# Kernel optimization log

Measured on AMD Instinct MI355X. Metric: run time of the kernel, lower is better.

## Reference

```python
import jax, jax.numpy as jnp
import numpy as np

NUM_HEADS = 16
KEY_DIM = 64
NUM_FEATURES = 256
D_MODEL = NUM_HEADS * KEY_DIM
EPS = 1e-6


def softmax_kernel(data, proj):
    # data: [..., N, D], proj: [D, F]
    # Faithful to source: ratio uses proj.shape[0] (=D), matching the TF code.
    data_normalizer = 1.0 / jnp.sqrt(jnp.sqrt(jnp.asarray(data.shape[-1], data.dtype)))
    ratio = 1.0 / jnp.sqrt(jnp.asarray(proj.shape[0], data.dtype))
    data = data_normalizer * data
    data_dash = jnp.einsum('...nd,df->...nf', data, proj)
    diag = jnp.sum(jnp.square(data), axis=-1, keepdims=True)  # [..., N, 1]
    return ratio * (jnp.exp(data_dash - diag / 2.0) + EPS)


def setup_inputs() -> dict:
    key = jax.random.key(0)
    ks = jax.random.split(key, 12)
    B, N = 4, 4096
    s = 1.0 / np.sqrt(D_MODEL)
    inp = {
        'queries': jax.random.normal(ks[0], (B, N, D_MODEL), jnp.float32),
        'keys': jax.random.normal(ks[1], (B, N, D_MODEL), jnp.float32),
        'Wq': jax.random.normal(ks[2], (D_MODEL, D_MODEL), jnp.float32) * s,
        'bq': jnp.zeros((D_MODEL,), jnp.float32),
        'Wk': jax.random.normal(ks[3], (D_MODEL, D_MODEL), jnp.float32) * s,
        'bk': jnp.zeros((D_MODEL,), jnp.float32),
        'Wv': jax.random.normal(ks[4], (D_MODEL, D_MODEL), jnp.float32) * s,
        'bv': jnp.zeros((D_MODEL,), jnp.float32),
        'Wo': jax.random.normal(ks[5], (D_MODEL, D_MODEL), jnp.float32) * s,
        'bo': jnp.zeros((D_MODEL,), jnp.float32),
        # GlorotNormal for [KEY_DIM, NUM_FEATURES]
        'proj': jax.random.normal(ks[6], (KEY_DIM, NUM_FEATURES), jnp.float32)
                * np.sqrt(2.0 / (KEY_DIM + NUM_FEATURES)),
    }
    return inp


def reference(queries, keys, Wq, bq, Wk, bk, Wv, bv, Wo, bo, proj):
    # Original code uses x = queries for q, k, v (self-attention); keys arg unused.
    x = queries
    B, N, _ = x.shape
    H, D = NUM_HEADS, KEY_DIM

    def split_heads(t):
        return t.reshape(B, N, H, D).transpose(0, 2, 1, 3)  # [B,H,N,D]

    q = split_heads(x @ Wq + bq)
    k = split_heads(x @ Wk + bk)
    v = split_heads(x @ Wv + bv)

    q_prime = softmax_kernel(q, proj)  # [B,H,N,F]
    k_prime = softmax_kernel(k, proj)  # [B,H,N,F]

    kv = jnp.einsum('bhnf,bhnd->bhfd', k_prime, v)        # [B,H,F,D]
    qkv = jnp.einsum('bhnf,bhfd->bhnd', q_prime, kv)       # [B,H,N,D]
    k_sum = jnp.sum(k_prime, axis=2)                        # [B,H,F]
    norm = jnp.einsum('bhnf,bhf->bhn', q_prime, k_sum) + EPS
    qkv = qkv / norm[..., None]

    out = qkv.transpose(0, 2, 1, 3).reshape(B, N, H * D)    # [B,N,d_model]
    return out @ Wo + bo
```

## Files before the change

### kernel.cpp

```cpp
#include <hip/hip_runtime.h>

typedef __attribute__((ext_vector_type(8))) short short8;
typedef __attribute__((ext_vector_type(4))) float f32x4;

#define MFMA16 __builtin_amdgcn_mfma_f32_16x16x32_bf16

#define GLOAD16(gp, lp) __builtin_amdgcn_global_load_lds(                      \
    (const __attribute__((address_space(1))) void*)(gp),                       \
    (__attribute__((address_space(3))) void*)(lp), 16, 0, 0)

__device__ __forceinline__ unsigned short f2bf(float f) {
  unsigned int u = __float_as_uint(f);
  unsigned int r = u + 0x7fffu + ((u >> 16) & 1u);
  return (unsigned short)(r >> 16);
}
__device__ __forceinline__ float bf2f(unsigned short h) {
  return __uint_as_float(((unsigned int)h) << 16);
}

__global__ __launch_bounds__(256) void cast_x_kernel(
    const float* __restrict__ in, unsigned short* __restrict__ out, int n4) {
  int i = blockIdx.x * 256 + threadIdx.x;
  if (i >= n4) return;
  float4 v = reinterpret_cast<const float4*>(in)[i];
  ushort4 o;
  o.x = f2bf(v.x); o.y = f2bf(v.y); o.z = f2bf(v.z); o.w = f2bf(v.w);
  reinterpret_cast<ushort4*>(out)[i] = o;
}

__global__ __launch_bounds__(256) void tcast_f32_kernel(
    const float* __restrict__ in, unsigned short* __restrict__ out, int R, int C) {
  __shared__ float t[64][65];
  int c0 = blockIdx.x * 64, r0 = blockIdx.y * 64;
  int tx = threadIdx.x, ty = threadIdx.y;
#pragma unroll
  for (int i = 0; i < 16; ++i)
    t[ty + 4 * i][tx] = in[(size_t)(r0 + ty + 4 * i) * C + c0 + tx];
  __syncthreads();
#pragma unroll
  for (int i = 0; i < 16; ++i)
    out[(size_t)(c0 + ty + 4 * i) * R + r0 + tx] = f2bf(t[tx][ty + 4 * i]);
}

__global__ __launch_bounds__(256) void t_bf16_kernel(
    const unsigned short* __restrict__ in, unsigned short* __restrict__ out, int R, int C) {
  __shared__ unsigned short t[64][66];
  size_t base = (size_t)blockIdx.z * (size_t)R * (size_t)C;
  int c0 = blockIdx.x * 64, r0 = blockIdx.y * 64;
  int tx = threadIdx.x, ty = threadIdx.y;
#pragma unroll
  for (int i = 0; i < 16; ++i)
    t[ty + 4 * i][tx] = in[base + (size_t)(r0 + ty + 4 * i) * C + c0 + tx];
  __syncthreads();
#pragma unroll
  for (int i = 0; i < 16; ++i)
    out[base + (size_t)(c0 + ty + 4 * i) * R + r0 + tx] = t[tx][ty + 4 * i];
}

template <int OUTF>
__global__ __launch_bounds__(256) void gemm_bt_kernel(
    const unsigned short* __restrict__ A,
    const unsigned short* W0, const unsigned short* W1, const unsigned short* W2,
    const float* b0, const float* b1, const float* b2,
    void* o0, void* o1, void* o2) {
  constexpr int KD = 1024, ND = 1024;
  const unsigned short* W = W0; const float* bias = b0; void* op = o0;
  if (blockIdx.z == 1) { W = W1; bias = b1; op = o1; }
  else if (blockIdx.z == 2) { W = W2; bias = b2; op = o2; }

  __shared__ unsigned short lsA[128 * 32];
  __shared__ unsigned short lsB[128 * 32];
  int tid = threadIdx.x;
  int w = tid >> 6, lane = tid & 63;
  int m0 = blockIdx.x * 128, n0 = blockIdx.y * 128;
  int wm = (w >> 1) * 64, wn = (w & 1) * 64;

  int srow0 = (w * 2 + 0) * 16 + (lane >> 2);
  int srow1 = (w * 2 + 1) * 16 + (lane >> 2);
  int scol = (lane & 3) * 8;
  const unsigned short* gA0 = A + (size_t)(m0 + srow0) * KD + scol;
  const unsigned short* gA1 = A + (size_t)(m0 + srow1) * KD + scol;
  const unsigned short* gB0 = W + (size_t)(n0 + srow0) * KD + scol;
  const unsigned short* gB1 = W + (size_t)(n0 + srow1) * KD + scol;
  unsigned short* lA0 = &lsA[(w * 2 + 0) * 512];
  unsigned short* lA1 = &lsA[(w * 2 + 1) * 512];
  unsigned short* lB0 = &lsB[(w * 2 + 0) * 512];
  unsigned short* lB1 = &lsB[(w * 2 + 1) * 512];

  f32x4 acc[4][4];
#pragma unroll
  for (int fm = 0; fm < 4; ++fm)
#pragma unroll
    for (int fn = 0; fn < 4; ++fn) acc[fm][fn] = (f32x4){0.f, 0.f, 0.f, 0.f};

  for (int kt = 0; kt < KD; kt += 32) {
    GLOAD16(gA0 + kt, lA0);
    GLOAD16(gA1 + kt, lA1);
    GLOAD16(gB0 + kt, lB0);
    GLOAD16(gB1 + kt, lB1);
    __syncthreads();
    short8 af[4], bfr[4];
#pragma unroll
    for (int fm = 0; fm < 4; ++fm)
      af[fm] = *reinterpret_cast<const short8*>(
          &lsA[(wm + fm * 16 + (lane & 15)) * 32 + (lane >> 4) * 8]);
#pragma unroll
    for (int fn = 0; fn < 4; ++fn)
      bfr[fn] = *reinterpret_cast<const short8*>(
          &lsB[(wn + fn * 16 + (lane & 15)) * 32 + (lane >> 4) * 8]);
#pragma unroll
    for (int fm = 0; fm < 4; ++fm)
#pragma unroll
      for (int fn = 0; fn < 4; ++fn)
        acc[fm][fn] = MFMA16(af[fm], bfr[fn], acc[fm][fn], 0, 0, 0);
    __syncthreads();
  }

#pragma unroll
  for (int fn = 0; fn < 4; ++fn) {
    int col = n0 + wn + fn * 16 + (lane & 15);
    float bv = bias[col];
#pragma unroll
    for (int fm = 0; fm < 4; ++fm) {
#pragma unroll
      for (int j = 0; j < 4; ++j) {
        int row = m0 + wm + fm * 16 + (lane >> 4) * 4 + j;
        float v = acc[fm][fn][j] + bv;
        if (OUTF)
          reinterpret_cast<float*>(op)[(size_t)row * ND + col] = v;
        else
          reinterpret_cast<unsigned short*>(op)[(size_t)row * ND + col] = f2bf(v);
      }
    }
  }
}

__global__ __launch_bounds__(256) void kv_fused_kernel(
    const unsigned short* __restrict__ K, const unsigned short* __restrict__ PT,
    const unsigned short* __restrict__ VT,
    float* __restrict__ kvp, float* __restrict__ ksp) {
  __shared__ unsigned short kp[256 * 40];
  int s = blockIdx.x, bh = blockIdx.y, b = bh >> 4, h = bh & 15;
  int tid = threadIdx.x, w = tid >> 6, lane = tid & 63;
  int lo = lane & 15, hi = lane >> 4;
  int f0w = w * 64;

  short8 pb[4][2];
#pragma unroll
  for (int fn = 0; fn < 4; ++fn) {
    int f = f0w + fn * 16 + lo;
    pb[fn][0] = *reinterpret_cast<const short8*>(PT + (size_t)f * 64 + hi * 8);
    pb[fn][1] = *reinterpret_cast<const short8*>(PT + (size_t)f * 64 + 32 + hi * 8);
  }
  const unsigned short* vbase[4];
#pragma unroll
  for (int fn = 0; fn < 4; ++fn)
    vbase[fn] = VT + (size_t)(bh * 64 + fn * 16 + lo) * 4096;

  f32x4 acck[4][4];
#pragma unroll
  for (int fm = 0; fm < 4; ++fm)
#pragma unroll
    for (int fn = 0; fn < 4; ++fn) acck[fm][fn] = (f32x4){0.f, 0.f, 0.f, 0.f};
  float ks[4] = {0.f, 0.f, 0.f, 0.f};

  for (int c = 0; c < 16; ++c) {
    int n0 = s * 512 + c * 32;
    const unsigned short* Ab = K + (size_t)(b * 4096 + n0) * 1024 + h * 64;
    short8 af[2][2];
    float dp[2] = {0.f, 0.f};
#pragma unroll
    for (int fm = 0; fm < 2; ++fm)
#pragma unroll
      for (int kt = 0; kt < 2; ++kt) {
        af[fm][kt] = *reinterpret_cast<const short8*>(
            Ab + (size_t)(fm * 16 + lo) * 1024 + kt * 32 + hi * 8);
#pragma unroll
        for (int j = 0; j < 8; ++j) {
          float qv = bf2f((unsigned short)af[fm][kt][j]);
          dp[fm] += qv * qv;
        }
      }
#pragma unroll
    for (int fm = 0; fm < 2; ++fm) {
      dp[fm] += __shfl_xor(dp[fm], 16);
      dp[fm] += __shfl_xor(dp[fm], 32);
    }
    f32x4 accf[2][4];
#pragma unroll
    for (int fm = 0; fm < 2; ++fm)
#pragma unroll
      for (int fn = 0; fn < 4; ++fn) accf[fm][fn] = (f32x4){0.f, 0.f, 0.f, 0.f};
#pragma unroll
    for (int fn = 0; fn < 4; ++fn) {
      accf[0][fn] = MFMA16(af[0][0], pb[fn][0], accf[0][fn], 0, 0, 0);
      accf[0][fn] = MFMA16(af[0][1], pb[fn][1], accf[0][fn], 0, 0, 0);
      accf[1][fn] = MFMA16(af[1][0], pb[fn][0], accf[1][fn], 0, 0, 0);
      accf[1][fn] = MFMA16(af[1][1], pb[fn][1], accf[1][fn], 0, 0, 0);
    }
#pragma unroll
    for (int fm = 0; fm < 2; ++fm)
#pragma unroll
      for (int fn = 0; fn < 4; ++fn)
#pragma unroll
        for (int j = 0; j < 4; ++j) {
          float dg = __shfl(dp[fm], hi * 4 + j);
          float v = 0.125f *
                    (__expf(0.35355339059327373f * accf[fm][fn][j] - 0.0625f * dg) + 1e-6f);
          ks[fn] += v;
          kp[(f0w + fn * 16 + lo) * 40 + fm * 16 + hi * 4 + j] = f2bf(v);
        }
    short8 a2[4], b2[4];
#pragma unroll
    for (int fm = 0; fm < 4; ++fm)
      a2[fm] = *reinterpret_cast<const short8*>(&kp[(f0w + fm * 16 + lo) * 40 + hi * 8]);
#pragma unroll
    for (int fn = 0; fn < 4; ++fn)
      b2[fn] = *reinterpret_cast<const short8*>(vbase[fn] + n0 + hi * 8);
#pragma unroll
    for (int fm = 0; fm < 4; ++fm)
#pragma unroll
      for (int fn = 0; fn < 4; ++fn)
        acck[fm][fn] = MFMA16(a2[fm], b2[fn], acck[fm][fn], 0, 0, 0);
  }
#pragma unroll
  for (int fn = 0; fn < 4; ++fn) {
    float v = ks[fn];
    v += __shfl_xor(v, 16);
    v += __shfl_xor(v, 32);
    if (hi == 0)
      ksp[(size_t)(s * 64 + bh) * 256 + f0w + fn * 16 + lo] = v;
  }
#pragma unroll
  for (int fm = 0; fm < 4; ++fm)
#pragma unroll
    for (int fn = 0; fn < 4; ++fn)
#pragma unroll
      for (int j = 0; j < 4; ++j)
        kvp[((size_t)(s * 64 + bh) * 256 + f0w + fm * 16 + hi * 4 + j) * 64 + fn * 16 + lo] =
            acck[fm][fn][j];
}

__global__ __launch_bounds__(256) void kvred_kernel(
    const float* __restrict__ kvp, const float* __restrict__ ksp,
    unsigned short* __restrict__ kvT, float* __restrict__ ksum) {
  int bh = blockIdx.x, tid = threadIdx.x;
  for (int i = tid; i < 64 * 256; i += 256) {
    int f = i >> 6, d = i & 63;
    float sum = 0.f;
#pragma unroll
    for (int s = 0; s < 8; ++s)
      sum += kvp[((size_t)(s * 64 + bh) * 256 + f) * 64 + d];
    kvT[(size_t)(bh * 64 + d) * 256 + f] = f2bf(sum);
  }
  {
    float t = 0.f;
#pragma unroll
    for (int s = 0; s < 8; ++s) t += ksp[(size_t)(s * 64 + bh) * 256 + tid];
    ksum[bh * 256 + tid] = t;
  }
}

__global__ __launch_bounds__(256) void qkv_fused_kernel(
    const unsigned short* __restrict__ Q, const unsigned short* __restrict__ PT,
    const unsigned short* __restrict__ KVT, const float* __restrict__ KSUM,
    unsigned short* __restrict__ Y) {
  __shared__ unsigned short qp[128 * 256];
  int bh = blockIdx.y, b = bh >> 4, h = bh & 15;
  int t0 = blockIdx.x * 128;
  int tid = threadIdx.x, w = tid >> 6, lane = tid & 63;
  int lo = lane & 15, hi = lane >> 4;
  int r0 = w * 32;
  const unsigned short* Ab = Q + (size_t)(b * 4096 + t0 + r0) * 1024 + h * 64;

  float ksr[16];
#pragma unroll
  for (int fn = 0; fn < 16; ++fn) ksr[fn] = KSUM[bh * 256 + fn * 16 + lo];

  short8 af[2][2];
  float dp[2] = {0.f, 0.f};
#pragma unroll
  for (int fm = 0; fm < 2; ++fm)
#pragma unroll
    for (int kt = 0; kt < 2; ++kt) {
      af[fm][kt] = *reinterpret_cast<const short8*>(
          Ab + (size_t)(fm * 16 + lo) * 1024 + kt * 32 + hi * 8);
#pragma unroll
      for (int j = 0; j < 8; ++j) {
        float qv = bf2f((unsigned short)af[fm][kt][j]);
        dp[fm] += qv * qv;
      }
    }
#pragma unroll
  for (int fm = 0; fm < 2; ++fm) {
    dp[fm] += __shfl_xor(dp[fm], 16);
    dp[fm] += __shfl_xor(dp[fm], 32);
  }

  float np[2][4] = {{0.f, 0.f, 0.f, 0.f}, {0.f, 0.f, 0.f, 0.f}};
#pragma unroll
  for (int hf = 0; hf < 2; ++hf) {
    f32x4 accf[2][8];
#pragma unroll
    for (int fm = 0; fm < 2; ++fm)
#pragma unroll
      for (int fn = 0; fn < 8; ++fn) accf[fm][fn] = (f32x4){0.f, 0.f, 0.f, 0.f};
#pragma unroll
    for (int fn = 0; fn < 8; ++fn) {
      int f = (hf * 8 + fn) * 16 + lo;
      short8 pb0 = *reinterpret_cast<const short8*>(PT + (size_t)f * 64 + hi * 8);
      short8 pb1 = *reinterpret_cast<const short8*>(PT + (size_t)f * 64 + 32 + hi * 8);
      accf[0][fn] = MFMA16(af[0][0], pb0, accf[0][fn], 0, 0, 0);
      accf[0][fn] = MFMA16(af[0][1], pb1, accf[0][fn], 0, 0, 0);
      accf[1][fn] = MFMA16(af[1][0], pb0, accf[1][fn], 0, 0, 0);
      accf[1][fn] = MFMA16(af[1][1], pb1, accf[1][fn], 0, 0, 0);
    }
#pragma unroll
    for (int fm = 0; fm < 2; ++fm)
#pragma unroll
      for (int fn = 0; fn < 8; ++fn)
#pragma unroll
        for (int j = 0; j < 4; ++j) {
          float dg = __shfl(dp[fm], hi * 4 + j);
          float v = 0.125f *
                    (__expf(0.35355339059327373f * accf[fm][fn][j] - 0.0625f * dg) + 1e-6f);
          np[fm][j] += v * ksr[hf * 8 + fn];
          int row = r0 + fm * 16 + hi * 4 + j;
          int f = (hf * 8 + fn) * 16 + lo;
          int byt = (row * 512 + f * 2) ^ ((row & 7) << 4);
          *reinterpret_cast<unsigned short*>(reinterpret_cast<char*>(qp) + byt) = f2bf(v);
        }
  }
#pragma unroll
  for (int fm = 0; fm < 2; ++fm)
#pragma unroll
    for (int j = 0; j < 4; ++j) {
      np[fm][j] += __shfl_xor(np[fm][j], 1);
      np[fm][j] += __shfl_xor(np[fm][j], 2);
      np[fm][j] += __shfl_xor(np[fm][j], 4);
      np[fm][j] += __shfl_xor(np[fm][j], 8);
    }
  f32x4 acco[2][4];
#pragma unroll
  for (int fm = 0; fm < 2; ++fm)
#pragma unroll
    for (int fn = 0; fn < 4; ++fn) acco[fm][fn] = (f32x4){0.f, 0.f, 0.f, 0.f};
#pragma unroll
  for (int kt2 = 0; kt2 < 8; ++kt2) {
    short8 a2[2], b2[4];
#pragma unroll
    for (int fm = 0; fm < 2; ++fm) {
      int row = r0 + fm * 16 + lo;
      int byt = (row * 512 + kt2 * 64 + hi * 16) ^ ((row & 7) << 4);
      a2[fm] = *reinterpret_cast<const short8*>(reinterpret_cast<char*>(qp) + byt);
    }
#pragma unroll
    for (int fn = 0; fn < 4; ++fn)
      b2[fn] = *reinterpret_cast<const short8*>(
          KVT + (size_t)(bh * 64 + fn * 16 + lo) * 256 + kt2 * 32 + hi * 8);
#pragma unroll
    for (int fm = 0; fm < 2; ++fm)
#pragma unroll
      for (int fn = 0; fn < 4; ++fn)
        acco[fm][fn] = MFMA16(a2[fm], b2[fn], acco[fm][fn], 0, 0, 0);
  }
#pragma unroll
  for (int fm = 0; fm < 2; ++fm)
#pragma unroll
    for (int j = 0; j < 4; ++j) {
      float nv = np[fm][j] + 1e-6f;
      int row = b * 4096 + t0 + r0 + fm * 16 + hi * 4 + j;
#pragma unroll
      for (int fn = 0; fn < 4; ++fn)
        Y[(size_t)row * 1024 + h * 64 + fn * 16 + lo] = f2bf(acco[fm][fn][j] / nv);
    }
}

extern "C" void kernel_launch(void* const* d_in, const int* in_sizes, int n_in,
                              void* d_out, int out_size, void* d_ws, size_t ws_size,
                              hipStream_t stream) {
  (void)in_sizes; (void)n_in; (void)out_size; (void)ws_size;
  const float* x    = (const float*)d_in[0];
  const float* Wq   = (const float*)d_in[2];
  const float* bq   = (const float*)d_in[3];
  const float* Wk   = (const float*)d_in[4];
  const float* bk   = (const float*)d_in[5];
  const float* Wv   = (const float*)d_in[6];
  const float* bv   = (const float*)d_in[7];
  const float* Wo   = (const float*)d_in[8];
  const float* bo   = (const float*)d_in[9];
  const float* proj = (const float*)d_in[10];
  float* out = (float*)d_out;

  constexpr size_t SZ_XB = (size_t)16384 * 1024 * 2;
  constexpr size_t SZ_W  = (size_t)1024 * 1024 * 2;
  constexpr size_t SZ_PT = (size_t)256 * 64 * 2;

  char* p = (char*)d_ws;
  size_t off = 0;
  char* a_xb  = p + off; off += SZ_XB;
  char* a_WqT = p + off; off += SZ_W;
  char* a_WkT = p + off; off += SZ_W;
  char* a_WvT = p + off; off += SZ_W;
  char* a_WoT = p + off; off += SZ_W;
  char* a_pT  = p + off; off += SZ_PT;
  char* a_qb  = p + off; off += SZ_XB;
  char* a_kb  = p + off; off += SZ_XB;
  char* a_ksp  = p + off; off += (size_t)8 * 64 * 256 * 4;
  char* a_kvT  = p + off; off += (size_t)64 * 64 * 256 * 2;
  char* a_ksum = p + off; off += (size_t)64 * 256 * 4;

  char* a_kvp = a_xb;
  char* a_y = a_kb;
  char* a_vb = (char*)d_out;
  char* a_vT = (char*)d_out + SZ_XB;

  dim3 tb(64, 4);

  cast_x_kernel<<<16384, 256, 0, stream>>>(x, (unsigned short*)a_xb, 16384 * 1024 / 4);
  tcast_f32_kernel<<<dim3(16, 16), tb, 0, stream>>>(Wq, (unsigned short*)a_WqT, 1024, 1024);
  tcast_f32_kernel<<<dim3(16, 16), tb, 0, stream>>>(Wk, (unsigned short*)a_WkT, 1024, 1024);
  tcast_f32_kernel<<<dim3(16, 16), tb, 0, stream>>>(Wv, (unsigned short*)a_WvT, 1024, 1024);
  tcast_f32_kernel<<<dim3(16, 16), tb, 0, stream>>>(Wo, (unsigned short*)a_WoT, 1024, 1024);
  tcast_f32_kernel<<<dim3(4, 1), tb, 0, stream>>>(proj, (unsigned short*)a_pT, 64, 256);

  gemm_bt_kernel<0><<<dim3(128, 8, 3), 256, 0, stream>>>(
      (unsigned short*)a_xb,
      (unsigned short*)a_WqT, (unsigned short*)a_WkT, (unsigned short*)a_WvT,
      bq, bk, bv, a_qb, a_kb, a_vb);

  t_bf16_kernel<<<dim3(16, 64, 4), tb, 0, stream>>>(
      (unsigned short*)a_vb, (unsigned short*)a_vT, 4096, 1024);

  kv_fused_kernel<<<dim3(8, 64), 256, 0, stream>>>(
      (unsigned short*)a_kb, (unsigned short*)a_pT, (unsigned short*)a_vT,
      (float*)a_kvp, (float*)a_ksp);
  kvred_kernel<<<64, 256, 0, stream>>>(
      (float*)a_kvp, (float*)a_ksp, (unsigned short*)a_kvT, (float*)a_ksum);

  qkv_fused_kernel<<<dim3(32, 64), 256, 0, stream>>>(
      (unsigned short*)a_qb, (unsigned short*)a_pT, (unsigned short*)a_kvT,
      (float*)a_ksum, (unsigned short*)a_y);

  gemm_bt_kernel<1><<<dim3(128, 8, 1), 256, 0, stream>>>(
      (unsigned short*)a_y,
      (unsigned short*)a_WoT, nullptr, nullptr,
      bo, nullptr, nullptr, out, nullptr, nullptr);
}
```

Measured before the change: 356.4 us.

## Rewrite projection GEMMs as 256x256 double-buffered tiles with swizzled LDS

Replaces the 128x128, single-buffered GEMM with a 256x256 tile per 512-thread block and a K-step of 64. LDS is double-buffered so the next tile's global->LDS loads overlap the current MFMAs. An XOR swizzle on LDS chunks avoids bank conflicts, and explicit waitcnt, barriers and setprio control the schedule. This is meant to raise operand reuse and hide memory latency in the QKV and output projections. The cost is much more LDS (128 KB) and registers per block, so occupancy drops, and only 256 or 768 blocks are launched.

```diff
diff --git a/kernel.cpp b/kernel.cpp
--- a/kernel.cpp
+++ b/kernel.cpp
@@ -58,80 +58,112 @@
 }
 
 template <int OUTF>
-__global__ __launch_bounds__(256) void gemm_bt_kernel(
+__global__ __launch_bounds__(512) void gemm256_kernel(
     const unsigned short* __restrict__ A,
     const unsigned short* W0, const unsigned short* W1, const unsigned short* W2,
     const float* b0, const float* b1, const float* b2,
     void* o0, void* o1, void* o2) {
-  constexpr int KD = 1024, ND = 1024;
+  constexpr int KD = 1024, ND = 1024, NT = KD / 64;
   const unsigned short* W = W0; const float* bias = b0; void* op = o0;
   if (blockIdx.z == 1) { W = W1; bias = b1; op = o1; }
   else if (blockIdx.z == 2) { W = W2; bias = b2; op = o2; }
 
-  __shared__ unsigned short lsA[128 * 32];
-  __shared__ unsigned short lsB[128 * 32];
+  __shared__ unsigned short lsA[2][16384];
+  __shared__ unsigned short lsB[2][16384];
   int tid = threadIdx.x;
   int w = tid >> 6, lane = tid & 63;
-  int m0 = blockIdx.x * 128, n0 = blockIdx.y * 128;
-  int wm = (w >> 1) * 64, wn = (w & 1) * 64;
-
-  int srow0 = (w * 2 + 0) * 16 + (lane >> 2);
-  int srow1 = (w * 2 + 1) * 16 + (lane >> 2);
-  int scol = (lane & 3) * 8;
-  const unsigned short* gA0 = A + (size_t)(m0 + srow0) * KD + scol;
-  const unsigned short* gA1 = A + (size_t)(m0 + srow1) * KD + scol;
-  const unsigned short* gB0 = W + (size_t)(n0 + srow0) * KD + scol;
-  const unsigned short* gB1 = W + (size_t)(n0 + srow1) * KD + scol;
-  unsigned short* lA0 = &lsA[(w * 2 + 0) * 512];
-  unsigned short* lA1 = &lsA[(w * 2 + 1) * 512];
-  unsigned short* lB0 = &lsB[(w * 2 + 0) * 512];
-  unsigned short* lB1 = &lsB[(w * 2 + 1) * 512];
-
-  f32x4 acc[4][4];
-#pragma unroll
-  for (int fm = 0; fm < 4; ++fm)
-#pragma unroll
-    for (int fn = 0; fn < 4; ++fn) acc[fm][fn] = (f32x4){0.f, 0.f, 0.f, 0.f};
-
-  for (int kt = 0; kt < KD; kt += 32) {
-    GLOAD16(gA0 + kt, lA0);
-    GLOAD16(gA1 + kt, lA1);
-    GLOAD16(gB0 + kt, lB0);
-    GLOAD16(gB1 + kt, lB1);
-    __syncthreads();
-    short8 af[4], bfr[4];
-#pragma unroll
-    for (int fm = 0; fm < 4; ++fm)
-      af[fm] = *reinterpret_cast<const short8*>(
-          &lsA[(wm + fm * 16 + (lane & 15)) * 32 + (lane >> 4) * 8]);
+  int lo = lane & 15, hi = lane >> 4;
+  int wr = w >> 2, wc = w & 3;
+  int m0 = blockIdx.x * 256, n0 = blockIdx.y * 256;
+
+  int srow = tid >> 3;
+  int schunk = (tid & 7) ^ (srow & 7);
+  const unsigned short* gA0 = A + (size_t)(m0 + srow) * KD + schunk * 8;
+  const unsigned short* gB0 = W + (size_t)(n0 + srow) * KD + schunk * 8;
+
+  f32x4 acc[8][4];
+#pragma unroll
+  for (int m = 0; m < 8; ++m)
+#pragma unroll
+    for (int fn = 0; fn < 4; ++fn) acc[m][fn] = (f32x4){0.f, 0.f, 0.f, 0.f};
+
+#pragma unroll
+  for (int i = 0; i < 4; ++i)
+    GLOAD16(gA0 + (size_t)i * 64 * KD, &lsA[0][i * 4096 + w * 512]);
+#pragma unroll
+  for (int i = 0; i < 4; ++i)
+    GLOAD16(gB0 + (size_t)i * 64 * KD, &lsB[0][i * 4096 + w * 512]);
+
+  for (int t = 0; t < NT; ++t) {
+    int buf = t & 1;
+    if (t < NT - 1) {
+      int kb = (t + 1) * 64;
+#pragma unroll
+      for (int i = 0; i < 4; ++i)
+        GLOAD16(gA0 + (size_t)i * 64 * KD + kb, &lsA[buf ^ 1][i * 4096 + w * 512]);
+#pragma unroll
+      for (int i = 0; i < 4; ++i)
+        GLOAD16(gB0 + (size_t)i * 64 * KD + kb, &lsB[buf ^ 1][i * 4096 + w * 512]);
+      __builtin_amdgcn_sched_barrier(0);
+      asm volatile("s_waitcnt vmcnt(8)" ::: "memory");
+    } else {
+      __builtin_amdgcn_sched_barrier(0);
+      asm volatile("s_waitcnt vmcnt(0)" ::: "memory");
+    }
+    __builtin_amdgcn_sched_barrier(0);
+    __builtin_amdgcn_s_barrier();
+    __builtin_amdgcn_sched_barrier(0);
+
+    short8 bfr[4][2];
 #pragma unroll
     for (int fn = 0; fn < 4; ++fn)
-      bfr[fn] = *reinterpret_cast<const short8*>(
-          &lsB[(wn + fn * 16 + (lane & 15)) * 32 + (lane >> 4) * 8]);
-#pragma unroll
-    for (int fm = 0; fm < 4; ++fm)
-#pragma unroll
-      for (int fn = 0; fn < 4; ++fn)
-        acc[fm][fn] = MFMA16(af[fm], bfr[fn], acc[fm][fn], 0, 0, 0);
-    __syncthreads();
+#pragma unroll
+      for (int ks = 0; ks < 2; ++ks) {
+        int col = wc * 64 + fn * 16 + lo;
+        bfr[fn][ks] = *reinterpret_cast<const short8*>(
+            &lsB[buf][col * 64 + ((ks * 4 + hi) ^ (lo & 7)) * 8]);
+      }
+    __builtin_amdgcn_s_setprio(1);
+#pragma unroll
+    for (int mp = 0; mp < 4; ++mp) {
+      short8 afr[2][2];
+#pragma unroll
+      for (int mi = 0; mi < 2; ++mi)
+#pragma unroll
+        for (int ks = 0; ks < 2; ++ks) {
+          int row = wr * 128 + mp * 32 + mi * 16 + lo;
+          afr[mi][ks] = *reinterpret_cast<const short8*>(
+              &lsA[buf][row * 64 + ((ks * 4 + hi) ^ (lo & 7)) * 8]);
+        }
+#pragma unroll
+      for (int mi = 0; mi < 2; ++mi)
+#pragma unroll
+        for (int fn = 0; fn < 4; ++fn) {
+          acc[mp * 2 + mi][fn] = MFMA16(afr[mi][0], bfr[fn][0], acc[mp * 2 + mi][fn], 0, 0, 0);
+          acc[mp * 2 + mi][fn] = MFMA16(afr[mi][1], bfr[fn][1], acc[mp * 2 + mi][fn], 0, 0, 0);
+        }
+    }
+    __builtin_amdgcn_s_setprio(0);
+    __builtin_amdgcn_sched_barrier(0);
+    __builtin_amdgcn_s_barrier();
+    __builtin_amdgcn_sched_barrier(0);
   }
 
 #pragma unroll
   for (int fn = 0; fn < 4; ++fn) {
-    int col = n0 + wn + fn * 16 + (lane & 15);
+    int col = n0 + wc * 64 + fn * 16 + lo;
     float bv = bias[col];
 #pragma unroll
-    for (int fm = 0; fm < 4; ++fm) {
+    for (int m = 0; m < 8; ++m)
 #pragma unroll
       for (int j = 0; j < 4; ++j) {
-        int row = m0 + wm + fm * 16 + (lane >> 4) * 4 + j;
-        float v = acc[fm][fn][j] + bv;
+        int row = m0 + wr * 128 + m * 16 + hi * 4 + j;
+        float v = acc[m][fn][j] + bv;
         if (OUTF)
           reinterpret_cast<float*>(op)[(size_t)row * ND + col] = v;
         else
           reinterpret_cast<unsigned short*>(op)[(size_t)row * ND + col] = f2bf(v);
       }
-    }
   }
 }
 
@@ -424,7 +456,7 @@
   tcast_f32_kernel<<<dim3(16, 16), tb, 0, stream>>>(Wo, (unsigned short*)a_WoT, 1024, 1024);
   tcast_f32_kernel<<<dim3(4, 1), tb, 0, stream>>>(proj, (unsigned short*)a_pT, 64, 256);
 
-  gemm_bt_kernel<0><<<dim3(128, 8, 3), 256, 0, stream>>>(
+  gemm256_kernel<0><<<dim3(64, 4, 3), 512, 0, stream>>>(
       (unsigned short*)a_xb,
       (unsigned short*)a_WqT, (unsigned short*)a_WkT, (unsigned short*)a_WvT,
       bq, bk, bv, a_qb, a_kb, a_vb);
@@ -442,7 +474,7 @@
       (unsigned short*)a_qb, (unsigned short*)a_pT, (unsigned short*)a_kvT,
       (float*)a_ksum, (unsigned short*)a_y);
 
-  gemm_bt_kernel<1><<<dim3(128, 8, 1), 256, 0, stream>>>(
+  gemm256_kernel<1><<<dim3(64, 4, 1), 512, 0, stream>>>(
       (unsigned short*)a_y,
       (unsigned short*)a_WoT, nullptr, nullptr,
       bo, nullptr, nullptr, out, nullptr, nullptr);
```

Measured after the change: 353.4 us. No clear change (-0.8%).
